# Optimization experiments

Hardware: AMD Instinct MI355X
Metric: run time of the kernel (lower is better)

The kernel has to match this reference:

```python
import jax, jax.numpy as jnp
import numpy as np

B, TE, TD, H = 8, 512, 128, 256

def setup_inputs() -> dict:
    key = jax.random.key(0)
    k1, k2, k3, k4, k5 = jax.random.split(key, 5)
    return {
        "encoder_outputs": jax.random.normal(k1, (B, TE, H), dtype=jnp.float32),
        "decoder_outputs": jax.random.normal(k2, (B, TD, H), dtype=jnp.float32),
        "W_a": jax.random.normal(k3, (H, H), dtype=jnp.float32) * (1.0 / np.sqrt(H)),
        "U_a": jax.random.normal(k4, (H, H), dtype=jnp.float32) * (1.0 / np.sqrt(H)),
        "V_a": jax.random.normal(k5, (H, 1), dtype=jnp.float32) * (1.0 / np.sqrt(H)),
    }

def reference(encoder_outputs, decoder_outputs, W_a, U_a, V_a):
    # Bahdanau additive attention.
    enc_proj = jnp.einsum("beh,hk->bek", encoder_outputs, W_a)   # [B,TE,H]
    dec_proj = jnp.einsum("bdh,hk->bdk", decoder_outputs, U_a)   # [B,TD,H]
    # Broadcast add -> tanh -> project with V_a: [B,TD,TE]
    score = jnp.tanh(enc_proj[:, None, :, :] + dec_proj[:, :, None, :])  # [B,TD,TE,H]
    score = jnp.einsum("bdeh,h->bde", score, V_a[:, 0])          # [B,TD,TE]
    attention_weights = jax.nn.softmax(score, axis=-1)           # over encoder positions
    context = jnp.einsum("bde,beh->bdh", attention_weights, encoder_outputs)
    return (context, attention_weights)
```

## Files before the change

### kernel.cpp

```cpp
#include <hip/hip_runtime.h>
#include <hip/hip_bf16.h>

#ifndef __has_builtin
#define __has_builtin(x) 0
#endif

constexpr int B_ = 8, TE_ = 512, TD_ = 128, H_ = 256;
constexpr float TWO_LOG2E = 2.8853900817779268f;
constexpr float LOG2E = 1.4426950408889634f;

typedef float  vf2    __attribute__((ext_vector_type(2)));
typedef short  bf16x8 __attribute__((ext_vector_type(8)));
typedef float  f32x4  __attribute__((ext_vector_type(4)));

__device__ __forceinline__ float exp2_fast(float x) {
#if __has_builtin(__builtin_amdgcn_exp2f)
  return __builtin_amdgcn_exp2f(x);
#else
  return exp2f(x);
#endif
}
__device__ __forceinline__ float rcp_fast(float x) {
#if __has_builtin(__builtin_amdgcn_rcpf)
  return __builtin_amdgcn_rcpf(x);
#else
  return 1.0f / x;
#endif
}
__device__ __forceinline__ vf2 fma2(vf2 a, vf2 b, vf2 c) {
#if __has_builtin(__builtin_elementwise_fma)
  return __builtin_elementwise_fma(a, b, c);
#else
  vf2 r; r.x = __fmaf_rn(a.x, b.x, c.x); r.y = __fmaf_rn(a.y, b.y, c.y); return r;
#endif
}
__device__ __forceinline__ void bf16split(float x, unsigned short& hi, unsigned short& lo) {
  unsigned u = __float_as_uint(x);
  hi = (unsigned short)(u >> 16);
  float hif = __uint_as_float((unsigned)hi << 16);
  lo = (unsigned short)(__float_as_uint(x - hif) >> 16);
}

__global__ __launch_bounds__(256)
void proj_mfma(const float* __restrict__ enc, const float* __restrict__ dec,
               const float* __restrict__ W, const float* __restrict__ U,
               float* __restrict__ ep, float* __restrict__ dp) {
  __shared__ unsigned short Ah[32][40], Al[32][40], Bh[32][40], Bl[32][40];
  const int tid = threadIdx.x;
  const int mt = blockIdx.x;
  const int n0 = blockIdx.y * 32;
  const float* A; const float* Bm; float* C; int row0;
  if (mt < 128) { A = enc; Bm = W; C = ep; row0 = mt * 32; }
  else          { A = dec; Bm = U; C = dp; row0 = (mt - 128) * 32; }
  const int w = tid >> 6, lane = tid & 63;
  const int mw = (w & 1) * 16, nw = (w >> 1) * 16;
  const int quad = lane >> 4, l16 = lane & 15;
  const int am = tid >> 3, ak = (tid & 7) * 4;
  const int bn = tid & 31, bk = (tid >> 5) * 4;

  f32x4 acc = {0.f, 0.f, 0.f, 0.f};
  for (int k0 = 0; k0 < H_; k0 += 32) {
    float4 a4 = *(const float4*)&A[(long)(row0 + am) * H_ + k0 + ak];
    unsigned short h0, l0, h1, l1, h2, l2, h3, l3;
    bf16split(a4.x, h0, l0); bf16split(a4.y, h1, l1);
    bf16split(a4.z, h2, l2); bf16split(a4.w, h3, l3);
    *(ushort4*)&Ah[am][ak] = make_ushort4(h0, h1, h2, h3);
    *(ushort4*)&Al[am][ak] = make_ushort4(l0, l1, l2, l3);
    float b0 = Bm[(long)(k0 + bk + 0) * H_ + n0 + bn];
    float b1 = Bm[(long)(k0 + bk + 1) * H_ + n0 + bn];
    float b2 = Bm[(long)(k0 + bk + 2) * H_ + n0 + bn];
    float b3 = Bm[(long)(k0 + bk + 3) * H_ + n0 + bn];
    bf16split(b0, h0, l0); bf16split(b1, h1, l1);
    bf16split(b2, h2, l2); bf16split(b3, h3, l3);
    *(ushort4*)&Bh[bn][bk] = make_ushort4(h0, h1, h2, h3);
    *(ushort4*)&Bl[bn][bk] = make_ushort4(l0, l1, l2, l3);
    __syncthreads();
    bf16x8 ah = *(const bf16x8*)&Ah[mw + l16][quad * 8];
    bf16x8 al = *(const bf16x8*)&Al[mw + l16][quad * 8];
    bf16x8 bh = *(const bf16x8*)&Bh[nw + l16][quad * 8];
    bf16x8 bl = *(const bf16x8*)&Bl[nw + l16][quad * 8];
    acc = __builtin_amdgcn_mfma_f32_16x16x32_bf16(ah, bh, acc, 0, 0, 0);
    acc = __builtin_amdgcn_mfma_f32_16x16x32_bf16(ah, bl, acc, 0, 0, 0);
    acc = __builtin_amdgcn_mfma_f32_16x16x32_bf16(al, bh, acc, 0, 0, 0);
    __syncthreads();
  }
#pragma unroll
  for (int r = 0; r < 4; ++r)
    C[(long)(row0 + mw + quad * 4 + r) * H_ + n0 + nw + l16] =
        exp2_fast(acc[r] * TWO_LOG2E);
}

__global__ __launch_bounds__(256)
void score_kernel(const float* __restrict__ ep, const float* __restrict__ dp,
                  const float* __restrict__ v, float* __restrict__ sc) {
  __shared__ __align__(16) float eps[128][68];
  __shared__ __align__(16) float dps[16][68];
  __shared__ __align__(16) float vs[64];
  const int tid = threadIdx.x;
  const int bz = blockIdx.z;
  const int b = bz >> 1;
  const int h_lo = (bz & 1) * 128;
  const int e0 = blockIdx.x * 128;
  const int d0 = blockIdx.y * 16;
  const int w = tid >> 6;
  const int lane = tid & 63;

  vf2 acc[4][2];
#pragma unroll
  for (int j = 0; j < 4; ++j) {
    acc[j][0] = (vf2){0.f, 0.f};
    acc[j][1] = (vf2){0.f, 0.f};
  }

  for (int h0 = h_lo; h0 < h_lo + 128; h0 += 64) {
#pragma unroll
    for (int i = 0; i < 8; ++i) {
      int idx = tid + i * 256;
      int r = idx >> 4, c = (idx & 15) << 2;
      *(float4*)&eps[r][c] = *(const float4*)&ep[(long)(b * TE_ + e0 + r) * H_ + h0 + c];
    }
    {
      int r = tid >> 4, c = (tid & 15) << 2;
      *(float4*)&dps[r][c] = *(const float4*)&dp[(long)(b * TD_ + d0 + r) * H_ + h0 + c];
    }
    if (tid < 16) {
      float4 v4 = *(const float4*)&v[h0 + tid * 4];
      float4 o; o.x = -2.f * v4.x; o.y = -2.f * v4.y; o.z = -2.f * v4.z; o.w = -2.f * v4.w;
      *(float4*)&vs[tid * 4] = o;
    }
    __syncthreads();
    const vf2 one2 = {1.f, 1.f};
#pragma unroll 4
    for (int hh = 0; hh < 64; hh += 4) {
      float4 eaf = *(const float4*)&eps[lane][hh];
      float4 ebf = *(const float4*)&eps[lane + 64][hh];
      float4 vvf = *(const float4*)&vs[hh];
      vf2 ea0 = {eaf.x, eaf.y}, ea1 = {eaf.z, eaf.w};
      vf2 eb0 = {ebf.x, ebf.y}, eb1 = {ebf.z, ebf.w};
      vf2 vv0 = {vvf.x, vvf.y}, vv1 = {vvf.z, vvf.w};
#pragma unroll
      for (int j = 0; j < 4; ++j) {
        float4 df = *(const float4*)&dps[4 * w + j][hh];
        vf2 dd0 = {df.x, df.y}, dd1 = {df.z, df.w};
        vf2 t0 = fma2(ea0, dd0, one2);
        vf2 t1 = fma2(ea1, dd1, one2);
        vf2 u0 = fma2(eb0, dd0, one2);
        vf2 u1 = fma2(eb1, dd1, one2);
        vf2 r0, r1, s0, s1;
        r0.x = rcp_fast(t0.x); r0.y = rcp_fast(t0.y);
        r1.x = rcp_fast(t1.x); r1.y = rcp_fast(t1.y);
        s0.x = rcp_fast(u0.x); s0.y = rcp_fast(u0.y);
        s1.x = rcp_fast(u1.x); s1.y = rcp_fast(u1.y);
        acc[j][0] = fma2(vv0, r0, acc[j][0]); acc[j][0] = fma2(vv1, r1, acc[j][0]);
        acc[j][1] = fma2(vv0, s0, acc[j][1]); acc[j][1] = fma2(vv1, s1, acc[j][1]);
      }
    }
    __syncthreads();
  }
  long rbase = ((long)(bz & 1) * B_ * TD_ + (long)b * TD_ + d0 + 4 * w) * TE_ + e0 + lane;
#pragma unroll
  for (int j = 0; j < 4; ++j) {
    sc[rbase + (long)j * TE_]      = acc[j][0].x + acc[j][0].y;
    sc[rbase + (long)j * TE_ + 64] = acc[j][1].x + acc[j][1].y;
  }
}

__global__ __launch_bounds__(64)
void softmax_kernel(const float* __restrict__ sc, float* __restrict__ attn) {
  const long row = blockIdx.x;
  const float* p0 = sc + row * TE_;
  const float* p1 = sc + ((long)B_ * TD_ + row) * TE_;
  float* pout = attn + row * TE_;
  const int t = threadIdx.x;
  float x[8];
  float m = -1e30f;
#pragma unroll
  for (int k = 0; k < 8; ++k) {
    x[k] = p0[t + 64 * k] + p1[t + 64 * k];
    m = fmaxf(m, x[k]);
  }
#pragma unroll
  for (int off = 32; off; off >>= 1) m = fmaxf(m, __shfl_xor(m, off, 64));
  float s = 0.f;
#pragma unroll
  for (int k = 0; k < 8; ++k) { x[k] = exp2_fast((x[k] - m) * LOG2E); s += x[k]; }
#pragma unroll
  for (int off = 32; off; off >>= 1) s += __shfl_xor(s, off, 64);
  const float r = rcp_fast(s);
#pragma unroll
  for (int k = 0; k < 8; ++k) pout[t + 64 * k] = x[k] * r;
}

__global__ __launch_bounds__(256)
void ctx_mfma(const float* __restrict__ attn, const float* __restrict__ enc,
              float* __restrict__ ctx) {
  __shared__ unsigned short Ah[32][40], Al[32][40], Bh[32][40], Bl[32][40];
  const int tid = threadIdx.x;
  const int m0 = blockIdx.x * 32;
  const int n0 = blockIdx.y * 32;
  const int b = blockIdx.z;
  const float* A = attn + (long)b * TD_ * TE_;
  const float* E = enc + (long)b * TE_ * H_;
  const int w = tid >> 6, lane = tid & 63;
  const int mw = (w & 1) * 16, nw = (w >> 1) * 16;
  const int quad = lane >> 4, l16 = lane & 15;
  const int am = tid >> 3, ak = (tid & 7) * 4;
  const int bn = tid & 31, bk = (tid >> 5) * 4;

  f32x4 acc = {0.f, 0.f, 0.f, 0.f};
  for (int k0 = 0; k0 < TE_; k0 += 32) {
    float4 a4 = *(const float4*)&A[(long)(m0 + am) * TE_ + k0 + ak];
    unsigned short h0, l0, h1, l1, h2, l2, h3, l3;
    bf16split(a4.x, h0, l0); bf16split(a4.y, h1, l1);
    bf16split(a4.z, h2, l2); bf16split(a4.w, h3, l3);
    *(ushort4*)&Ah[am][ak] = make_ushort4(h0, h1, h2, h3);
    *(ushort4*)&Al[am][ak] = make_ushort4(l0, l1, l2, l3);
    float b0 = E[(long)(k0 + bk + 0) * H_ + n0 + bn];
    float b1 = E[(long)(k0 + bk + 1) * H_ + n0 + bn];
    float b2 = E[(long)(k0 + bk + 2) * H_ + n0 + bn];
    float b3 = E[(long)(k0 + bk + 3) * H_ + n0 + bn];
    bf16split(b0, h0, l0); bf16split(b1, h1, l1);
    bf16split(b2, h2, l2); bf16split(b3, h3, l3);
    *(ushort4*)&Bh[bn][bk] = make_ushort4(h0, h1, h2, h3);
    *(ushort4*)&Bl[bn][bk] = make_ushort4(l0, l1, l2, l3);
    __syncthreads();
    bf16x8 ah = *(const bf16x8*)&Ah[mw + l16][quad * 8];
    bf16x8 al = *(const bf16x8*)&Al[mw + l16][quad * 8];
    bf16x8 bh = *(const bf16x8*)&Bh[nw + l16][quad * 8];
    bf16x8 bl = *(const bf16x8*)&Bl[nw + l16][quad * 8];
    acc = __builtin_amdgcn_mfma_f32_16x16x32_bf16(ah, bh, acc, 0, 0, 0);
    acc = __builtin_amdgcn_mfma_f32_16x16x32_bf16(ah, bl, acc, 0, 0, 0);
    acc = __builtin_amdgcn_mfma_f32_16x16x32_bf16(al, bh, acc, 0, 0, 0);
    __syncthreads();
  }
#pragma unroll
  for (int r = 0; r < 4; ++r)
    ctx[((long)b * TD_ + m0 + mw + quad * 4 + r) * H_ + n0 + nw + l16] = acc[r];
}

extern "C" void kernel_launch(void* const* d_in, const int* in_sizes, int n_in,
                              void* d_out, int out_size, void* d_ws, size_t ws_size,
                              hipStream_t stream) {
  const float* enc = (const float*)d_in[0];
  const float* dec = (const float*)d_in[1];
  const float* Wa  = (const float*)d_in[2];
  const float* Ua  = (const float*)d_in[3];
  const float* Va  = (const float*)d_in[4];

  float* out  = (float*)d_out;
  float* ctx  = out;
  float* attn = out + (long)B_ * TD_ * H_;

  float* ep = (float*)d_ws;
  float* dp = ep + (long)B_ * TE_ * H_;
  float* sc = dp + (long)B_ * TD_ * H_;

  proj_mfma<<<dim3(160, 8), 256, 0, stream>>>(enc, dec, Wa, Ua, ep, dp);
  score_kernel<<<dim3(TE_ / 128, TD_ / 16, 2 * B_), 256, 0, stream>>>(ep, dp, Va, sc);
  softmax_kernel<<<dim3(B_ * TD_), 64, 0, stream>>>(sc, attn);
  ctx_mfma<<<dim3(TD_ / 32, H_ / 32, B_), 256, 0, stream>>>(attn, enc, ctx);
}
```

Baseline: 102.0 us.

## Fuse score and softmax into row kernel with transposed encoder projection

The projection kernel now writes the encoder projection transposed as [B,H,TE], so a new row kernel can stream contiguous encoder rows straight from global memory with register double-buffering. Each row block handles 4 decoder rows across all 512 encoder positions, splits H across 8 waves, reduces the partial scores in shared memory and applies the softmax in place. This removes the separate softmax launch and the round trip of the split-H score buffer through global memory. In exchange the grid shrinks to 256 blocks of 512 threads, each using about 70KB of shared memory, which may cut occupancy.

```diff
diff --git a/kernel.cpp b/kernel.cpp
--- a/kernel.cpp
+++ b/kernel.cpp
@@ -44,14 +44,14 @@
 __global__ __launch_bounds__(256)
 void proj_mfma(const float* __restrict__ enc, const float* __restrict__ dec,
                const float* __restrict__ W, const float* __restrict__ U,
-               float* __restrict__ ep, float* __restrict__ dp) {
+               float* __restrict__ ept, float* __restrict__ dp) {
   __shared__ unsigned short Ah[32][40], Al[32][40], Bh[32][40], Bl[32][40];
   const int tid = threadIdx.x;
   const int mt = blockIdx.x;
   const int n0 = blockIdx.y * 32;
-  const float* A; const float* Bm; float* C; int row0;
-  if (mt < 128) { A = enc; Bm = W; C = ep; row0 = mt * 32; }
-  else          { A = dec; Bm = U; C = dp; row0 = (mt - 128) * 32; }
+  const float* A; const float* Bm; int row0;
+  if (mt < 128) { A = enc; Bm = W; row0 = mt * 32; }
+  else          { A = dec; Bm = U; row0 = (mt - 128) * 32; }
   const int w = tid >> 6, lane = tid & 63;
   const int mw = (w & 1) * 16, nw = (w >> 1) * 16;
   const int quad = lane >> 4, l16 = lane & 15;
@@ -84,111 +84,140 @@
     acc = __builtin_amdgcn_mfma_f32_16x16x32_bf16(al, bh, acc, 0, 0, 0);
     __syncthreads();
   }
-#pragma unroll
-  for (int r = 0; r < 4; ++r)
-    C[(long)(row0 + mw + quad * 4 + r) * H_ + n0 + nw + l16] =
-        exp2_fast(acc[r] * TWO_LOG2E);
-}
-
-__global__ __launch_bounds__(256)
-void score_kernel(const float* __restrict__ ep, const float* __restrict__ dp,
-                  const float* __restrict__ v, float* __restrict__ sc) {
-  __shared__ __align__(16) float eps[128][68];
-  __shared__ __align__(16) float dps[16][68];
-  __shared__ __align__(16) float vs[64];
+  if (mt < 128) {
+    const int b = row0 >> 9;
+    const int e0 = (row0 & 511) + mw;
+    const int hcol = n0 + nw + l16;
+#pragma unroll
+    for (int r = 0; r < 4; ++r)
+      ept[((long)b * H_ + hcol) * TE_ + e0 + quad * 4 + r] =
+          exp2_fast(acc[r] * TWO_LOG2E);
+  } else {
+#pragma unroll
+    for (int r = 0; r < 4; ++r)
+      dp[(long)(row0 + mw + quad * 4 + r) * H_ + n0 + nw + l16] =
+          exp2_fast(acc[r] * TWO_LOG2E);
+  }
+}
+
+__global__ __launch_bounds__(512)
+void row_kernel(const float* __restrict__ ept, const float* __restrict__ dp,
+                const float* __restrict__ v, float* __restrict__ attn) {
+  __shared__ __align__(16) float d_s[4][256];
+  __shared__ __align__(16) float vs[256];
+  __shared__ __align__(16) float sc_part[8][4][512];
   const int tid = threadIdx.x;
-  const int bz = blockIdx.z;
-  const int b = bz >> 1;
-  const int h_lo = (bz & 1) * 128;
-  const int e0 = blockIdx.x * 128;
-  const int d0 = blockIdx.y * 16;
-  const int w = tid >> 6;
-  const int lane = tid & 63;
-
-  vf2 acc[4][2];
+  const int w = tid >> 6, lane = tid & 63;
+  const int b = blockIdx.y;
+  const int d0 = blockIdx.x * 4;
+
+  if (tid < 256) {
+    int r = tid >> 6, c = (tid & 63) << 2;
+    *(float4*)&d_s[r][c] = *(const float4*)&dp[(long)(b * TD_ + d0 + r) * H_ + c];
+  } else if (tid < 320) {
+    int i = tid - 256;
+    float4 v4 = *(const float4*)&v[i << 2];
+    float4 o; o.x = -2.f * v4.x; o.y = -2.f * v4.y; o.z = -2.f * v4.z; o.w = -2.f * v4.w;
+    *(float4*)&vs[i << 2] = o;
+  }
+  __syncthreads();
+
+  const float* ebase = ept + (long)b * H_ * TE_;
+  const int hbase = w * 32;
+  const int el = lane << 2;
+
+  vf2 acc[4][4];
+#pragma unroll
+  for (int d = 0; d < 4; ++d)
+#pragma unroll
+    for (int p = 0; p < 4; ++p) acc[d][p] = (vf2){0.f, 0.f};
+
+  const vf2 one2 = {1.f, 1.f};
+  float4 ea[4], eb[4];
 #pragma unroll
   for (int j = 0; j < 4; ++j) {
-    acc[j][0] = (vf2){0.f, 0.f};
-    acc[j][1] = (vf2){0.f, 0.f};
-  }
-
-  for (int h0 = h_lo; h0 < h_lo + 128; h0 += 64) {
-#pragma unroll
-    for (int i = 0; i < 8; ++i) {
-      int idx = tid + i * 256;
-      int r = idx >> 4, c = (idx & 15) << 2;
-      *(float4*)&eps[r][c] = *(const float4*)&ep[(long)(b * TE_ + e0 + r) * H_ + h0 + c];
+    ea[j] = *(const float4*)&ebase[(long)(hbase + j) * TE_ + el];
+    eb[j] = *(const float4*)&ebase[(long)(hbase + j) * TE_ + 256 + el];
+  }
+  for (int h = hbase; h < hbase + 32; h += 4) {
+    const int hn = (h + 4 < hbase + 32) ? h + 4 : hbase;
+    float4 na[4], nb[4];
+#pragma unroll
+    for (int j = 0; j < 4; ++j) {
+      na[j] = *(const float4*)&ebase[(long)(hn + j) * TE_ + el];
+      nb[j] = *(const float4*)&ebase[(long)(hn + j) * TE_ + 256 + el];
     }
-    {
-      int r = tid >> 4, c = (tid & 15) << 2;
-      *(float4*)&dps[r][c] = *(const float4*)&dp[(long)(b * TD_ + d0 + r) * H_ + h0 + c];
-    }
-    if (tid < 16) {
-      float4 v4 = *(const float4*)&v[h0 + tid * 4];
-      float4 o; o.x = -2.f * v4.x; o.y = -2.f * v4.y; o.z = -2.f * v4.z; o.w = -2.f * v4.w;
-      *(float4*)&vs[tid * 4] = o;
-    }
-    __syncthreads();
-    const vf2 one2 = {1.f, 1.f};
-#pragma unroll 4
-    for (int hh = 0; hh < 64; hh += 4) {
-      float4 eaf = *(const float4*)&eps[lane][hh];
-      float4 ebf = *(const float4*)&eps[lane + 64][hh];
-      float4 vvf = *(const float4*)&vs[hh];
-      vf2 ea0 = {eaf.x, eaf.y}, ea1 = {eaf.z, eaf.w};
-      vf2 eb0 = {ebf.x, ebf.y}, eb1 = {ebf.z, ebf.w};
-      vf2 vv0 = {vvf.x, vvf.y}, vv1 = {vvf.z, vvf.w};
+    float4 vv = *(const float4*)&vs[h];
+#pragma unroll
+    for (int d = 0; d < 4; ++d) {
+      float4 dd = *(const float4*)&d_s[d][h];
 #pragma unroll
       for (int j = 0; j < 4; ++j) {
-        float4 df = *(const float4*)&dps[4 * w + j][hh];
-        vf2 dd0 = {df.x, df.y}, dd1 = {df.z, df.w};
-        vf2 t0 = fma2(ea0, dd0, one2);
-        vf2 t1 = fma2(ea1, dd1, one2);
-        vf2 u0 = fma2(eb0, dd0, one2);
-        vf2 u1 = fma2(eb1, dd1, one2);
-        vf2 r0, r1, s0, s1;
+        float ddj = (j == 0) ? dd.x : (j == 1) ? dd.y : (j == 2) ? dd.z : dd.w;
+        float vvj = (j == 0) ? vv.x : (j == 1) ? vv.y : (j == 2) ? vv.z : vv.w;
+        vf2 dd2 = {ddj, ddj}, vv2 = {vvj, vvj};
+        float4 A4 = ea[j], B4 = eb[j];
+        vf2 t0 = fma2((vf2){A4.x, A4.y}, dd2, one2);
+        vf2 t1 = fma2((vf2){A4.z, A4.w}, dd2, one2);
+        vf2 t2 = fma2((vf2){B4.x, B4.y}, dd2, one2);
+        vf2 t3 = fma2((vf2){B4.z, B4.w}, dd2, one2);
+        vf2 r0, r1, r2, r3;
         r0.x = rcp_fast(t0.x); r0.y = rcp_fast(t0.y);
         r1.x = rcp_fast(t1.x); r1.y = rcp_fast(t1.y);
-        s0.x = rcp_fast(u0.x); s0.y = rcp_fast(u0.y);
-        s1.x = rcp_fast(u1.x); s1.y = rcp_fast(u1.y);
-        acc[j][0] = fma2(vv0, r0, acc[j][0]); acc[j][0] = fma2(vv1, r1, acc[j][0]);
-        acc[j][1] = fma2(vv0, s0, acc[j][1]); acc[j][1] = fma2(vv1, s1, acc[j][1]);
+        r2.x = rcp_fast(t2.x); r2.y = rcp_fast(t2.y);
+        r3.x = rcp_fast(t3.x); r3.y = rcp_fast(t3.y);
+        acc[d][0] = fma2(vv2, r0, acc[d][0]);
+        acc[d][1] = fma2(vv2, r1, acc[d][1]);
+        acc[d][2] = fma2(vv2, r2, acc[d][2]);
+        acc[d][3] = fma2(vv2, r3, acc[d][3]);
       }
     }
-    __syncthreads();
-  }
-  long rbase = ((long)(bz & 1) * B_ * TD_ + (long)b * TD_ + d0 + 4 * w) * TE_ + e0 + lane;
-#pragma unroll
-  for (int j = 0; j < 4; ++j) {
-    sc[rbase + (long)j * TE_]      = acc[j][0].x + acc[j][0].y;
-    sc[rbase + (long)j * TE_ + 64] = acc[j][1].x + acc[j][1].y;
-  }
-}
-
-__global__ __launch_bounds__(64)
-void softmax_kernel(const float* __restrict__ sc, float* __restrict__ attn) {
-  const long row = blockIdx.x;
-  const float* p0 = sc + row * TE_;
-  const float* p1 = sc + ((long)B_ * TD_ + row) * TE_;
-  float* pout = attn + row * TE_;
-  const int t = threadIdx.x;
-  float x[8];
-  float m = -1e30f;
-#pragma unroll
-  for (int k = 0; k < 8; ++k) {
-    x[k] = p0[t + 64 * k] + p1[t + 64 * k];
-    m = fmaxf(m, x[k]);
-  }
-#pragma unroll
-  for (int off = 32; off; off >>= 1) m = fmaxf(m, __shfl_xor(m, off, 64));
-  float s = 0.f;
-#pragma unroll
-  for (int k = 0; k < 8; ++k) { x[k] = exp2_fast((x[k] - m) * LOG2E); s += x[k]; }
-#pragma unroll
-  for (int off = 32; off; off >>= 1) s += __shfl_xor(s, off, 64);
-  const float r = rcp_fast(s);
-#pragma unroll
-  for (int k = 0; k < 8; ++k) pout[t + 64 * k] = x[k] * r;
+#pragma unroll
+    for (int j = 0; j < 4; ++j) { ea[j] = na[j]; eb[j] = nb[j]; }
+  }
+
+#pragma unroll
+  for (int d = 0; d < 4; ++d) {
+    float4 s0; s0.x = acc[d][0].x; s0.y = acc[d][0].y; s0.z = acc[d][1].x; s0.w = acc[d][1].y;
+    float4 s1; s1.x = acc[d][2].x; s1.y = acc[d][2].y; s1.z = acc[d][3].x; s1.w = acc[d][3].y;
+    *(float4*)&sc_part[w][d][el] = s0;
+    *(float4*)&sc_part[w][d][256 + el] = s1;
+  }
+  __syncthreads();
+
+  {
+    const int d = tid >> 7, e4 = (tid & 127) << 2;
+    float4 s = *(const float4*)&sc_part[0][d][e4];
+#pragma unroll
+    for (int sl = 1; sl < 8; ++sl) {
+      float4 q = *(const float4*)&sc_part[sl][d][e4];
+      s.x += q.x; s.y += q.y; s.z += q.z; s.w += q.w;
+    }
+    *(float4*)&sc_part[0][d][e4] = s;
+  }
+  __syncthreads();
+
+  if (w < 4) {
+    float4 x0 = *(const float4*)&sc_part[0][w][el];
+    float4 x1 = *(const float4*)&sc_part[0][w][256 + el];
+    float x[8] = {x0.x, x0.y, x0.z, x0.w, x1.x, x1.y, x1.z, x1.w};
+    float m = x[0];
+#pragma unroll
+    for (int k = 1; k < 8; ++k) m = fmaxf(m, x[k]);
+#pragma unroll
+    for (int off = 32; off; off >>= 1) m = fmaxf(m, __shfl_xor(m, off, 64));
+    float s = 0.f;
+#pragma unroll
+    for (int k = 0; k < 8; ++k) { x[k] = exp2_fast((x[k] - m) * LOG2E); s += x[k]; }
+#pragma unroll
+    for (int off = 32; off; off >>= 1) s += __shfl_xor(s, off, 64);
+    const float r = rcp_fast(s);
+    float* po = attn + ((long)b * TD_ + d0 + w) * TE_;
+    float4 o0; o0.x = x[0] * r; o0.y = x[1] * r; o0.z = x[2] * r; o0.w = x[3] * r;
+    float4 o1; o1.x = x[4] * r; o1.y = x[5] * r; o1.z = x[6] * r; o1.w = x[7] * r;
+    *(float4*)&po[el] = o0;
+    *(float4*)&po[256 + el] = o1;
+  }
 }
 
 __global__ __launch_bounds__(256)
@@ -251,12 +280,10 @@
   float* ctx  = out;
   float* attn = out + (long)B_ * TD_ * H_;
 
-  float* ep = (float*)d_ws;
-  float* dp = ep + (long)B_ * TE_ * H_;
-  float* sc = dp + (long)B_ * TD_ * H_;
-
-  proj_mfma<<<dim3(160, 8), 256, 0, stream>>>(enc, dec, Wa, Ua, ep, dp);
-  score_kernel<<<dim3(TE_ / 128, TD_ / 16, 2 * B_), 256, 0, stream>>>(ep, dp, Va, sc);
-  softmax_kernel<<<dim3(B_ * TD_), 64, 0, stream>>>(sc, attn);
+  float* ept = (float*)d_ws;
+  float* dp  = ept + (long)B_ * H_ * TE_;
+
+  proj_mfma<<<dim3(160, 8), 256, 0, stream>>>(enc, dec, Wa, Ua, ept, dp);
+  row_kernel<<<dim3(TD_ / 4, B_), 512, 0, stream>>>(ept, dp, Va, attn);
   ctx_mfma<<<dim3(TD_ / 32, H_ / 32, B_), 256, 0, stream>>>(attn, enc, ctx);
 }
```

New measurement: 105.5 us. +3.5%, slower.
